# Performance work log

Measured on AMD Instinct MI355X. Metric: run time of the kernel, lower is better.

## Reference

```python
import jax, jax.numpy as jnp
import numpy as np

B, Q, V, H, U = 4, 256, 2048, 512, 128

def setup_inputs() -> dict:
    key = jax.random.key(0)
    ks = jax.random.split(key, 5)
    return {
        "queries": jax.random.normal(ks[0], (B, Q, H), dtype=jnp.float32),
        "values": jax.random.normal(ks[1], (B, V, H), dtype=jnp.float32),
        "w1": jax.random.normal(ks[2], (H, U), dtype=jnp.float32) / np.sqrt(H),
        "w2": jax.random.normal(ks[3], (H, U), dtype=jnp.float32) / np.sqrt(H),
        "v": jax.random.normal(ks[4], (U,), dtype=jnp.float32) / np.sqrt(U),
    }

def reference(queries, values, w1, w2, v):
    # Project queries and values first (cheap GEMMs), then broadcast-add.
    pq = jnp.einsum("bqh,hu->bqu", queries, w1)          # [B,Q,U]
    pv = jnp.einsum("bvh,hu->bvu", values, w2)           # [B,V,U]
    # added_qv: [B,Q,V,U] -- the large intermediate the original materializes
    scores = jnp.einsum("bqvu,u->bqv", jnp.tanh(pq[:, :, None, :] + pv[:, None, :, :]), v)
    attn = jax.nn.softmax(scores, axis=-1)               # softmax over V (last axis, as tf.nn.softmax)
    return jnp.einsum("bqv,bvh->bqh", attn, values)      # [B,Q,H]
```

## Files before the change

### kernel.cpp

```cpp
#include <hip/hip_runtime.h>

#define BB 4
#define QQ 256
#define VV 2048
#define HH 512
#define UU 128

#define C2E   2.8853900817779268f
#define LOG2E 1.4426950408889634f

__device__ __forceinline__ void fma4(float4& a, float s, const float4& w) {
    a.x = fmaf(s, w.x, a.x);
    a.y = fmaf(s, w.y, a.y);
    a.z = fmaf(s, w.z, a.z);
    a.w = fmaf(s, w.w, a.w);
}
__device__ __forceinline__ float2 rcp2(float2 x) {
    return make_float2(__builtin_amdgcn_rcpf(x.x), __builtin_amdgcn_rcpf(x.y));
}
__device__ __forceinline__ float2 mul2(float2 a, float2 b) { return make_float2(a.x*b.x, a.y*b.y); }
__device__ __forceinline__ float2 muls(float2 a, float s)  { return make_float2(a.x*s, a.y*s); }
__device__ __forceinline__ float2 fma2(float2 a, float2 b, float2 c) {
    return make_float2(fmaf(a.x, b.x, c.x), fmaf(a.y, b.y, c.y));
}
__device__ __forceinline__ float2 fmas(float2 a, float s, float2 c) {
    return make_float2(fmaf(a.x, s, c.x), fmaf(a.y, s, c.y));
}

__global__ __launch_bounds__(256) void proj_kernel(const float* __restrict__ queries,
                                                   const float* __restrict__ values,
                                                   const float* __restrict__ w1,
                                                   const float* __restrict__ w2,
                                                   float* __restrict__ pqI,
                                                   float* __restrict__ pvI,
                                                   float* __restrict__ denom) {
    __shared__ float smem[32 * 36 + 32 * 128];
    float (*As)[36] = (float(*)[36])smem;
    float* Ws = smem + 32 * 36;
    float (*Ls)[36] = (float(*)[36])smem;

    const int bid = blockIdx.x;
    const int tid = threadIdx.x;
    if (bid == 0) *(float4*)&denom[tid * 4] = make_float4(0.f, 0.f, 0.f, 0.f);

    const bool isv = (bid < 256);
    const float* A; const float* W; int b, r0, ROWS; float* Ob;
    if (isv) {
        b = bid >> 6; r0 = (bid & 63) * 32;
        A = values + ((size_t)(b * VV + r0)) * HH;  W = w2;
        Ob = pvI + (size_t)b * UU * VV;  ROWS = VV;
    } else {
        const int q = bid - 256;
        b = q >> 3; r0 = (q & 7) * 32;
        A = queries + ((size_t)(b * QQ + r0)) * HH; W = w1;
        Ob = pqI + (size_t)b * UU * QQ;  ROWS = QQ;
    }

    const int tx = tid & 31;
    const int ty = tid >> 5;
    float4 acc[4];
#pragma unroll
    for (int j = 0; j < 4; j++) acc[j] = make_float4(0.f, 0.f, 0.f, 0.f);

    for (int k0 = 0; k0 < HH; k0 += 32) {
        {
            const int r = tid >> 3, kk4 = (tid & 7) * 4;
            const float4 a = *(const float4*)&A[(size_t)r * HH + k0 + kk4];
            As[kk4 + 0][r] = a.x; As[kk4 + 1][r] = a.y;
            As[kk4 + 2][r] = a.z; As[kk4 + 3][r] = a.w;
        }
#pragma unroll
        for (int t = 0; t < 4; t++) {
            const int f = tid + t * 256;
            const int kk = f >> 5, u4 = (f & 31) * 4;
            *(float4*)&Ws[kk * 128 + u4] = *(const float4*)&W[(size_t)(k0 + kk) * UU + u4];
        }
        __syncthreads();
#pragma unroll
        for (int kk = 0; kk < 32; kk++) {
            const float4 a = *(const float4*)&As[kk][ty * 4];
            const float4 w = *(const float4*)&Ws[kk * 128 + tx * 4];
            fma4(acc[0], a.x, w);
            fma4(acc[1], a.y, w);
            fma4(acc[2], a.z, w);
            fma4(acc[3], a.w, w);
        }
        __syncthreads();
    }
#pragma unroll
    for (int j = 0; j < 4; j++) {
        const float aa[4] = {acc[j].x, acc[j].y, acc[j].z, acc[j].w};
#pragma unroll
        for (int i = 0; i < 4; i++)
            Ls[tx * 4 + i][ty * 4 + j] = __builtin_amdgcn_exp2f(aa[i] * C2E);
    }
    __syncthreads();
#pragma unroll
    for (int t = 0; t < 4; t++) {
        const int idx = tid + t * 256;
        const int g = idx >> 5, r = idx & 31;
        float4 o;
        o.x = Ls[4 * g + 0][r]; o.y = Ls[4 * g + 1][r];
        o.z = Ls[4 * g + 2][r]; o.w = Ls[4 * g + 3][r];
        *(float4*)&Ob[((size_t)g * ROWS + r0 + r) * 4] = o;
    }
}

__global__ __launch_bounds__(512, 6) void fused_kernel(const float* __restrict__ pqI,
                                                       const float* __restrict__ pvI,
                                                       const float* __restrict__ vvec,
                                                       const float* __restrict__ values,
                                                       float* __restrict__ slab,
                                                       float* __restrict__ denom) {
    __shared__ float att[256][16];
    __shared__ float scratch[16][512];
    __shared__ float wred[4][16];
    const int tid = threadIdx.x;
    const int bid = blockIdx.x;
    const int vs = bid & 7, qb = (bid >> 3) & 15, b = bid >> 7;
    const int qbase = qb * 16, vbase = vs * 256;

    const int vloc = tid & 255, uh = tid >> 8;
    const int v = vbase + vloc;

    float vsum = 0.0f;
#pragma unroll
    for (int u4 = 0; u4 < UU; u4 += 4) {
        const float4 t = *(const float4*)&vvec[u4];
        vsum += t.x + t.y + t.z + t.w;
    }

    const float* pv4 = pvI + (size_t)b * UU * VV + (size_t)v * 4;
    const float* pq4 = pqI + (size_t)b * UU * QQ + (size_t)qbase * 4;

    float2 acc[8];
#pragma unroll
    for (int p = 0; p < 8; p++) acc[p] = make_float2(0.f, 0.f);

    const int G0 = uh * 16;
    float4 ev = *(const float4*)&pv4[(size_t)G0 * VV * 4];

    for (int g = 0; g < 16; g++) {
        const int G = G0 + g;
        const float* eqp = &pq4[(size_t)G * QQ * 4];
        float4 evn;
        if (g < 15) evn = *(const float4*)&pv4[(size_t)(G + 1) * VV * 4];
        const float4 wq = *(const float4*)&vvec[G * 4];
        const float w0 = 2.f * wq.x, w1 = 2.f * wq.y;
        const float w2 = 2.f * wq.z, w3 = 2.f * wq.w;
#pragma unroll
        for (int p = 0; p < 8; p++) {
            const float4 e0 = *(const float4*)&eqp[(2 * p) * 4];
            const float4 e1 = *(const float4*)&eqp[(2 * p + 1) * 4];
            const float2 a1 = make_float2(fmaf(e0.x, ev.x, 1.f), fmaf(e1.x, ev.x, 1.f));
            const float2 b1 = make_float2(fmaf(e0.y, ev.y, 1.f), fmaf(e1.y, ev.y, 1.f));
            const float2 c1 = make_float2(fmaf(e0.z, ev.z, 1.f), fmaf(e1.z, ev.z, 1.f));
            const float2 d1 = make_float2(fmaf(e0.w, ev.w, 1.f), fmaf(e1.w, ev.w, 1.f));
            const float2 pab = mul2(a1, b1), pcd = mul2(c1, d1);
            const float2 nab = fmas(a1, w1, muls(b1, w0));
            const float2 ncd = fmas(c1, w3, muls(d1, w2));
            const float2 num = fma2(nab, pcd, mul2(ncd, pab));
            const float2 den = mul2(pab, pcd);
            acc[p] = fma2(num, rcp2(den), acc[p]);
        }
        ev = evn;
    }

    float* cbuf = &scratch[0][0];
    if (uh == 1) {
#pragma unroll
        for (int p = 0; p < 8; p++)
            *(float2*)&cbuf[vloc * 16 + 2 * p] = acc[p];
    }
    __syncthreads();
    if (uh == 0) {
#pragma unroll
        for (int p = 0; p < 8; p++) {
            const float2 hi = *(const float2*)&cbuf[vloc * 16 + 2 * p];
            float2 e;
            e.x = __builtin_amdgcn_exp2f((vsum - (acc[p].x + hi.x)) * LOG2E);
            e.y = __builtin_amdgcn_exp2f((vsum - (acc[p].y + hi.y)) * LOG2E);
            att[vloc][2 * p + 0] = e.x;
            att[vloc][2 * p + 1] = e.y;
            acc[p] = e;
        }
#pragma unroll
        for (int off = 1; off < 64; off <<= 1) {
#pragma unroll
            for (int p = 0; p < 8; p++) {
                acc[p].x += __shfl_xor(acc[p].x, off, 64);
                acc[p].y += __shfl_xor(acc[p].y, off, 64);
            }
        }
        if ((tid & 63) == 0) {
            const int w = tid >> 6;
#pragma unroll
            for (int p = 0; p < 8; p++) {
                wred[w][2 * p + 0] = acc[p].x;
                wred[w][2 * p + 1] = acc[p].y;
            }
        }
    }
    __syncthreads();
    if (tid < 16)
        atomicAdd(&denom[b * QQ + qbase + tid],
                  wred[0][tid] + wred[1][tid] + wred[2][tid] + wred[3][tid]);

    const int hg = tid & 127, sel = tid >> 7;
    const int qh = sel & 1, vh = sel >> 1;
    const int h0 = hg * 4;
    const float* vp = values + ((size_t)(b * VV + vbase + vh * 128)) * HH + h0;

    float4 oacc[8];
#pragma unroll
    for (int j = 0; j < 8; j++) oacc[j] = make_float4(0.f, 0.f, 0.f, 0.f);

#pragma unroll 2
    for (int vv = 0; vv < 128; vv++) {
        const float4 w = *(const float4*)&vp[(size_t)vv * HH];
        const float4 a0 = *(const float4*)&att[vh * 128 + vv][qh * 8 + 0];
        const float4 a1 = *(const float4*)&att[vh * 128 + vv][qh * 8 + 4];
        fma4(oacc[0], a0.x, w); fma4(oacc[1], a0.y, w);
        fma4(oacc[2], a0.z, w); fma4(oacc[3], a0.w, w);
        fma4(oacc[4], a1.x, w); fma4(oacc[5], a1.y, w);
        fma4(oacc[6], a1.z, w); fma4(oacc[7], a1.w, w);
    }

    if (vh == 1) {
#pragma unroll
        for (int j = 0; j < 8; j++) *(float4*)&scratch[qh * 8 + j][h0] = oacc[j];
    }
    __syncthreads();
    if (vh == 0) {
        float* sp = slab + (size_t)vs * (BB * QQ * HH);
#pragma unroll
        for (int j = 0; j < 8; j++) {
            const float4 p4 = *(const float4*)&scratch[qh * 8 + j][h0];
            const int q = qh * 8 + j;
            float4 o;
            o.x = oacc[j].x + p4.x; o.y = oacc[j].y + p4.y;
            o.z = oacc[j].z + p4.z; o.w = oacc[j].w + p4.w;
            *(float4*)&sp[((size_t)(b * QQ + qbase + q)) * HH + h0] = o;
        }
    }
}

__global__ __launch_bounds__(256) void reduce_kernel(const float* __restrict__ slab,
                                                     const float* __restrict__ denom,
                                                     float* __restrict__ out) {
    const int i = blockIdx.x * 256 + threadIdx.x;
    const float r = __builtin_amdgcn_rcpf(denom[i >> 7]);
    const float4* s4 = (const float4*)slab;
    float4 s = s4[i];
#pragma unroll
    for (int k = 1; k < 8; k++) {
        const float4 p = s4[(size_t)k * (BB * QQ * HH / 4) + i];
        s.x += p.x; s.y += p.y; s.z += p.z; s.w += p.w;
    }
    s.x *= r; s.y *= r; s.z *= r; s.w *= r;
    ((float4*)out)[i] = s;
}

extern "C" void kernel_launch(void* const* d_in, const int* in_sizes, int n_in,
                              void* d_out, int out_size, void* d_ws, size_t ws_size,
                              hipStream_t stream) {
    const float* queries = (const float*)d_in[0];
    const float* values  = (const float*)d_in[1];
    const float* w1      = (const float*)d_in[2];
    const float* w2      = (const float*)d_in[3];
    const float* vvec    = (const float*)d_in[4];
    float* out = (float*)d_out;

    float* ws    = (float*)d_ws;
    float* pqI   = ws;
    float* pvI   = pqI + BB * UU * QQ;
    float* denom = pvI + (size_t)BB * UU * VV;
    float* slab  = denom + BB * QQ;

    proj_kernel<<<256 + 32, 256, 0, stream>>>(queries, values, w1, w2, pqI, pvI, denom);
    fused_kernel<<<BB * (QQ / 16) * (VV / 256), 512, 0, stream>>>(pqI, pvI, vvec, values, slab, denom);
    reduce_kernel<<<(BB * QQ * HH) / 4 / 256, 256, 0, stream>>>(slab, denom, out);
}
```

Before: 172.2 us.

## Double fused kernel block to 1024 threads, splitting queries and value rows

The fused block grows from 512 to 1024 threads. In the score phase the extra threads split the 16 queries into two halves of 8, and in the weighted-sum phase the value rows are split four ways instead of two. A three-way LDS reduction runs in two rounds that reuse one scratch buffer, and the partial-sum scratch layout moves to column-major to avoid bank conflicts. Each thread carries less work and fewer registers, which aims to hide latency with more waves, at the cost of more barriers and LDS traffic.

```diff
diff --git a/kernel.cpp b/kernel.cpp
--- a/kernel.cpp
+++ b/kernel.cpp
@@ -106,21 +106,23 @@
     }
 }
 
-__global__ __launch_bounds__(512, 6) void fused_kernel(const float* __restrict__ pqI,
-                                                       const float* __restrict__ pvI,
-                                                       const float* __restrict__ vvec,
-                                                       const float* __restrict__ values,
-                                                       float* __restrict__ slab,
-                                                       float* __restrict__ denom) {
-    __shared__ float att[256][16];
-    __shared__ float scratch[16][512];
-    __shared__ float wred[4][16];
+__global__ __launch_bounds__(1024, 8) void fused_kernel(const float* __restrict__ pqI,
+                                                        const float* __restrict__ pvI,
+                                                        const float* __restrict__ vvec,
+                                                        const float* __restrict__ values,
+                                                        float* __restrict__ slab,
+                                                        float* __restrict__ denom) {
+    __shared__ float att[256][20];
+    __shared__ float cscr[3 * 8 * 512];
+    __shared__ float wred[2][4][8];
     const int tid = threadIdx.x;
     const int bid = blockIdx.x;
     const int vs = bid & 7, qb = (bid >> 3) & 15, b = bid >> 7;
     const int qbase = qb * 16, vbase = vs * 256;
 
-    const int vloc = tid & 255, uh = tid >> 8;
+    const int vloc = tid & 255;
+    const int uh = (tid >> 8) & 1;
+    const int qhh = tid >> 9;
     const int v = vbase + vloc;
 
     float vsum = 0.0f;
@@ -131,25 +133,25 @@
     }
 
     const float* pv4 = pvI + (size_t)b * UU * VV + (size_t)v * 4;
-    const float* pq4 = pqI + (size_t)b * UU * QQ + (size_t)qbase * 4;
-
-    float2 acc[8];
-#pragma unroll
-    for (int p = 0; p < 8; p++) acc[p] = make_float2(0.f, 0.f);
+    const float* eqb = pqI + (size_t)b * UU * QQ + (size_t)(qbase + qhh * 8) * 4;
+
+    float2 acc[4];
+#pragma unroll
+    for (int p = 0; p < 4; p++) acc[p] = make_float2(0.f, 0.f);
 
     const int G0 = uh * 16;
     float4 ev = *(const float4*)&pv4[(size_t)G0 * VV * 4];
 
     for (int g = 0; g < 16; g++) {
         const int G = G0 + g;
-        const float* eqp = &pq4[(size_t)G * QQ * 4];
+        const float* eqp = &eqb[(size_t)G * QQ * 4];
         float4 evn;
         if (g < 15) evn = *(const float4*)&pv4[(size_t)(G + 1) * VV * 4];
         const float4 wq = *(const float4*)&vvec[G * 4];
         const float w0 = 2.f * wq.x, w1 = 2.f * wq.y;
         const float w2 = 2.f * wq.z, w3 = 2.f * wq.w;
 #pragma unroll
-        for (int p = 0; p < 8; p++) {
+        for (int p = 0; p < 4; p++) {
             const float4 e0 = *(const float4*)&eqp[(2 * p) * 4];
             const float4 e1 = *(const float4*)&eqp[(2 * p + 1) * 4];
             const float2 a1 = make_float2(fmaf(e0.x, ev.x, 1.f), fmaf(e1.x, ev.x, 1.f));
@@ -166,81 +168,93 @@
         ev = evn;
     }
 
-    float* cbuf = &scratch[0][0];
+    float* cb = &cscr[(size_t)qhh * 16 * 256];
     if (uh == 1) {
 #pragma unroll
-        for (int p = 0; p < 8; p++)
-            *(float2*)&cbuf[vloc * 16 + 2 * p] = acc[p];
+        for (int p = 0; p < 4; p++) {
+            cb[(2 * p + 0) * 256 + vloc] = acc[p].x;
+            cb[(2 * p + 1) * 256 + vloc] = acc[p].y;
+        }
     }
     __syncthreads();
     if (uh == 0) {
 #pragma unroll
-        for (int p = 0; p < 8; p++) {
-            const float2 hi = *(const float2*)&cbuf[vloc * 16 + 2 * p];
+        for (int p = 0; p < 4; p++) {
+            const float hx = cb[(2 * p + 0) * 256 + vloc];
+            const float hy = cb[(2 * p + 1) * 256 + vloc];
             float2 e;
-            e.x = __builtin_amdgcn_exp2f((vsum - (acc[p].x + hi.x)) * LOG2E);
-            e.y = __builtin_amdgcn_exp2f((vsum - (acc[p].y + hi.y)) * LOG2E);
-            att[vloc][2 * p + 0] = e.x;
-            att[vloc][2 * p + 1] = e.y;
+            e.x = __builtin_amdgcn_exp2f((vsum - (acc[p].x + hx)) * LOG2E);
+            e.y = __builtin_amdgcn_exp2f((vsum - (acc[p].y + hy)) * LOG2E);
+            *(float2*)&att[vloc][qhh * 8 + 2 * p] = e;
             acc[p] = e;
         }
 #pragma unroll
         for (int off = 1; off < 64; off <<= 1) {
 #pragma unroll
-            for (int p = 0; p < 8; p++) {
+            for (int p = 0; p < 4; p++) {
                 acc[p].x += __shfl_xor(acc[p].x, off, 64);
                 acc[p].y += __shfl_xor(acc[p].y, off, 64);
             }
         }
         if ((tid & 63) == 0) {
-            const int w = tid >> 6;
-#pragma unroll
-            for (int p = 0; p < 8; p++) {
-                wred[w][2 * p + 0] = acc[p].x;
-                wred[w][2 * p + 1] = acc[p].y;
+            const int vq = (tid >> 6) & 3;
+#pragma unroll
+            for (int p = 0; p < 4; p++) {
+                wred[qhh][vq][2 * p + 0] = acc[p].x;
+                wred[qhh][vq][2 * p + 1] = acc[p].y;
             }
         }
     }
     __syncthreads();
-    if (tid < 16)
+    if (tid < 16) {
+        const int qq = tid & 7, qh2 = tid >> 3;
         atomicAdd(&denom[b * QQ + qbase + tid],
-                  wred[0][tid] + wred[1][tid] + wred[2][tid] + wred[3][tid]);
+                  wred[qh2][0][qq] + wred[qh2][1][qq] + wred[qh2][2][qq] + wred[qh2][3][qq]);
+    }
 
     const int hg = tid & 127, sel = tid >> 7;
     const int qh = sel & 1, vh = sel >> 1;
     const int h0 = hg * 4;
-    const float* vp = values + ((size_t)(b * VV + vbase + vh * 128)) * HH + h0;
+    const float* vp = values + ((size_t)(b * VV + vbase + vh * 64)) * HH + h0;
 
     float4 oacc[8];
 #pragma unroll
     for (int j = 0; j < 8; j++) oacc[j] = make_float4(0.f, 0.f, 0.f, 0.f);
 
 #pragma unroll 2
-    for (int vv = 0; vv < 128; vv++) {
+    for (int vv = 0; vv < 64; vv++) {
         const float4 w = *(const float4*)&vp[(size_t)vv * HH];
-        const float4 a0 = *(const float4*)&att[vh * 128 + vv][qh * 8 + 0];
-        const float4 a1 = *(const float4*)&att[vh * 128 + vv][qh * 8 + 4];
+        const float4 a0 = *(const float4*)&att[vh * 64 + vv][qh * 8 + 0];
+        const float4 a1 = *(const float4*)&att[vh * 64 + vv][qh * 8 + 4];
         fma4(oacc[0], a0.x, w); fma4(oacc[1], a0.y, w);
         fma4(oacc[2], a0.z, w); fma4(oacc[3], a0.w, w);
         fma4(oacc[4], a1.x, w); fma4(oacc[5], a1.y, w);
         fma4(oacc[6], a1.z, w); fma4(oacc[7], a1.w, w);
     }
 
-    if (vh == 1) {
-#pragma unroll
-        for (int j = 0; j < 8; j++) *(float4*)&scratch[qh * 8 + j][h0] = oacc[j];
-    }
-    __syncthreads();
-    if (vh == 0) {
-        float* sp = slab + (size_t)vs * (BB * QQ * HH);
-#pragma unroll
-        for (int j = 0; j < 8; j++) {
-            const float4 p4 = *(const float4*)&scratch[qh * 8 + j][h0];
-            const int q = qh * 8 + j;
-            float4 o;
-            o.x = oacc[j].x + p4.x; o.y = oacc[j].y + p4.y;
-            o.z = oacc[j].z + p4.z; o.w = oacc[j].w + p4.w;
-            *(float4*)&sp[((size_t)(b * QQ + qbase + q)) * HH + h0] = o;
+    float (*scr)[512] = (float(*)[512])cscr;
+    for (int r = 0; r < 2; r++) {
+        __syncthreads();
+        if (qh == r && vh > 0) {
+#pragma unroll
+            for (int j = 0; j < 8; j++)
+                *(float4*)&scr[(vh - 1) * 8 + j][h0] = oacc[j];
+        }
+        __syncthreads();
+        if (qh == r && vh == 0) {
+            float* sp = slab + (size_t)vs * (BB * QQ * HH);
+#pragma unroll
+            for (int j = 0; j < 8; j++) {
+                const float4 p0 = *(const float4*)&scr[0 * 8 + j][h0];
+                const float4 p1 = *(const float4*)&scr[1 * 8 + j][h0];
+                const float4 p2 = *(const float4*)&scr[2 * 8 + j][h0];
+                float4 o;
+                o.x = oacc[j].x + p0.x + p1.x + p2.x;
+                o.y = oacc[j].y + p0.y + p1.y + p2.y;
+                o.z = oacc[j].z + p0.z + p1.z + p2.z;
+                o.w = oacc[j].w + p0.w + p1.w + p2.w;
+                *(float4*)&sp[((size_t)(b * QQ + qbase + r * 8 + j)) * HH + h0] = o;
+            }
         }
     }
 }
@@ -278,6 +292,6 @@
     float* slab  = denom + BB * QQ;
 
     proj_kernel<<<256 + 32, 256, 0, stream>>>(queries, values, w1, w2, pqI, pvI, denom);
-    fused_kernel<<<BB * (QQ / 16) * (VV / 256), 512, 0, stream>>>(pqI, pvI, vvec, values, slab, denom);
+    fused_kernel<<<BB * (QQ / 16) * (VV / 256), 1024, 0, stream>>>(pqI, pvI, vvec, values, slab, denom);
     reduce_kernel<<<(BB * QQ * HH) / 4 / 256, 256, 0, stream>>>(slab, denom, out);
 }
```

Measured after the change: 173.5 us. No clear change (+0.8%).

## Widen fused kernel to 512-value slices with 1024-thread blocks

Applied to the files above, without the earlier changes.

Each block of the fused kernel now covers 512 values instead of 256, with 1024 threads, so the grid halves to 256 blocks and only four partial-output slabs are written and summed in the reduce kernel. The partial-sum scratch is transposed to column-major to avoid LDS bank conflicts, and the attention rows are padded to 20 floats. The final cross-slice reduction now runs in two synchronized rounds over four value quarters. The aim is to cut slab write and reduce traffic and atomics. In exchange, 256 large blocks may underfill the GPU's compute units, and the extra barriers add cost.

```diff
diff --git a/kernel.cpp b/kernel.cpp
--- a/kernel.cpp
+++ b/kernel.cpp
@@ -106,21 +106,22 @@
     }
 }
 
-__global__ __launch_bounds__(512, 6) void fused_kernel(const float* __restrict__ pqI,
-                                                       const float* __restrict__ pvI,
-                                                       const float* __restrict__ vvec,
-                                                       const float* __restrict__ values,
-                                                       float* __restrict__ slab,
-                                                       float* __restrict__ denom) {
-    __shared__ float att[256][16];
-    __shared__ float scratch[16][512];
-    __shared__ float wred[4][16];
+__global__ __launch_bounds__(1024, 8) void fused_kernel(const float* __restrict__ pqI,
+                                                        const float* __restrict__ pvI,
+                                                        const float* __restrict__ vvec,
+                                                        const float* __restrict__ values,
+                                                        float* __restrict__ slab,
+                                                        float* __restrict__ denom) {
+    __shared__ float att[512][20];
+    __shared__ float scratch[24 * 512];
+    __shared__ float wred[8][16];
     const int tid = threadIdx.x;
     const int bid = blockIdx.x;
-    const int vs = bid & 7, qb = (bid >> 3) & 15, b = bid >> 7;
-    const int qbase = qb * 16, vbase = vs * 256;
-
-    const int vloc = tid & 255, uh = tid >> 8;
+    const int vs = bid & 3, qb = (bid >> 2) & 15, b = bid >> 6;
+    const int qbase = qb * 16, vbase = vs * 512;
+
+    const int vloc = tid & 511;
+    const int uh = tid >> 9;
     const int v = vbase + vloc;
 
     float vsum = 0.0f;
@@ -166,22 +167,24 @@
         ev = evn;
     }
 
-    float* cbuf = &scratch[0][0];
+    float* cb = scratch;
     if (uh == 1) {
 #pragma unroll
-        for (int p = 0; p < 8; p++)
-            *(float2*)&cbuf[vloc * 16 + 2 * p] = acc[p];
+        for (int p = 0; p < 8; p++) {
+            cb[(2 * p + 0) * 512 + vloc] = acc[p].x;
+            cb[(2 * p + 1) * 512 + vloc] = acc[p].y;
+        }
     }
     __syncthreads();
     if (uh == 0) {
 #pragma unroll
         for (int p = 0; p < 8; p++) {
-            const float2 hi = *(const float2*)&cbuf[vloc * 16 + 2 * p];
+            const float hx = cb[(2 * p + 0) * 512 + vloc];
+            const float hy = cb[(2 * p + 1) * 512 + vloc];
             float2 e;
-            e.x = __builtin_amdgcn_exp2f((vsum - (acc[p].x + hi.x)) * LOG2E);
-            e.y = __builtin_amdgcn_exp2f((vsum - (acc[p].y + hi.y)) * LOG2E);
-            att[vloc][2 * p + 0] = e.x;
-            att[vloc][2 * p + 1] = e.y;
+            e.x = __builtin_amdgcn_exp2f((vsum - (acc[p].x + hx)) * LOG2E);
+            e.y = __builtin_amdgcn_exp2f((vsum - (acc[p].y + hy)) * LOG2E);
+            *(float2*)&att[vloc][2 * p] = e;
             acc[p] = e;
         }
 #pragma unroll
@@ -202,9 +205,12 @@
         }
     }
     __syncthreads();
-    if (tid < 16)
-        atomicAdd(&denom[b * QQ + qbase + tid],
-                  wred[0][tid] + wred[1][tid] + wred[2][tid] + wred[3][tid]);
+    if (tid < 16) {
+        float s = 0.f;
+#pragma unroll
+        for (int w = 0; w < 8; w++) s += wred[w][tid];
+        atomicAdd(&denom[b * QQ + qbase + tid], s);
+    }
 
     const int hg = tid & 127, sel = tid >> 7;
     const int qh = sel & 1, vh = sel >> 1;
@@ -226,21 +232,29 @@
         fma4(oacc[6], a1.z, w); fma4(oacc[7], a1.w, w);
     }
 
-    if (vh == 1) {
-#pragma unroll
-        for (int j = 0; j < 8; j++) *(float4*)&scratch[qh * 8 + j][h0] = oacc[j];
-    }
-    __syncthreads();
-    if (vh == 0) {
-        float* sp = slab + (size_t)vs * (BB * QQ * HH);
-#pragma unroll
-        for (int j = 0; j < 8; j++) {
-            const float4 p4 = *(const float4*)&scratch[qh * 8 + j][h0];
-            const int q = qh * 8 + j;
-            float4 o;
-            o.x = oacc[j].x + p4.x; o.y = oacc[j].y + p4.y;
-            o.z = oacc[j].z + p4.z; o.w = oacc[j].w + p4.w;
-            *(float4*)&sp[((size_t)(b * QQ + qbase + q)) * HH + h0] = o;
+    float (*scr)[512] = (float(*)[512])scratch;
+    for (int r = 0; r < 2; r++) {
+        __syncthreads();
+        if (qh == r && vh > 0) {
+#pragma unroll
+            for (int j = 0; j < 8; j++)
+                *(float4*)&scr[(vh - 1) * 8 + j][h0] = oacc[j];
+        }
+        __syncthreads();
+        if (qh == r && vh == 0) {
+            float* sp = slab + (size_t)vs * (BB * QQ * HH);
+#pragma unroll
+            for (int j = 0; j < 8; j++) {
+                const float4 p0 = *(const float4*)&scr[0 * 8 + j][h0];
+                const float4 p1 = *(const float4*)&scr[1 * 8 + j][h0];
+                const float4 p2 = *(const float4*)&scr[2 * 8 + j][h0];
+                float4 o;
+                o.x = oacc[j].x + p0.x + p1.x + p2.x;
+                o.y = oacc[j].y + p0.y + p1.y + p2.y;
+                o.z = oacc[j].z + p0.z + p1.z + p2.z;
+                o.w = oacc[j].w + p0.w + p1.w + p2.w;
+                *(float4*)&sp[((size_t)(b * QQ + qbase + r * 8 + j)) * HH + h0] = o;
+            }
         }
     }
 }
@@ -253,7 +267,7 @@
     const float4* s4 = (const float4*)slab;
     float4 s = s4[i];
 #pragma unroll
-    for (int k = 1; k < 8; k++) {
+    for (int k = 1; k < 4; k++) {
         const float4 p = s4[(size_t)k * (BB * QQ * HH / 4) + i];
         s.x += p.x; s.y += p.y; s.z += p.z; s.w += p.w;
     }
@@ -278,6 +292,6 @@
     float* slab  = denom + BB * QQ;
 
     proj_kernel<<<256 + 32, 256, 0, stream>>>(queries, values, w1, w2, pqI, pvI, denom);
-    fused_kernel<<<BB * (QQ / 16) * (VV / 256), 512, 0, stream>>>(pqI, pvI, vvec, values, slab, denom);
+    fused_kernel<<<BB * (QQ / 16) * (VV / 512), 1024, 0, stream>>>(pqI, pvI, vvec, values, slab, denom);
     reduce_kernel<<<(BB * QQ * HH) / 4 / 256, 256, 0, stream>>>(slab, denom, out);
 }
```

Result: no change. 173.8 us (+0.9%).
